# Optimization experiments

Measured on AMD Instinct MI355X. Metric: run time of the kernel, lower is better.

The kernel has to match this reference:

```python
import jax, jax.numpy as jnp
import numpy as np

N_NODES = 50000
E_EDGES = 1600000
D = 256


def setup_inputs() -> dict:
    key = jax.random.key(0)
    ks = jax.random.split(key, 10)
    inp = {
        "x": jax.random.normal(ks[0], (N_NODES, D), dtype=jnp.float32),
        "W0": jax.random.normal(ks[1], (D, D), dtype=jnp.float32) * (1.0 / np.sqrt(D)),
        "W1": jax.random.normal(ks[2], (D, D), dtype=jnp.float32) * (1.0 / np.sqrt(D)),
        "b": jnp.zeros((D,), dtype=jnp.float32),
        "src0": jax.random.randint(ks[3], (E_EDGES,), 0, N_NODES, dtype=jnp.int32),
        "dst0": jax.random.randint(ks[4], (E_EDGES,), 0, N_NODES, dtype=jnp.int32),
        "val0": jax.random.uniform(ks[5], (E_EDGES,), dtype=jnp.float32),
        "src1": jax.random.randint(ks[6], (E_EDGES,), 0, N_NODES, dtype=jnp.int32),
        "dst1": jax.random.randint(ks[7], (E_EDGES,), 0, N_NODES, dtype=jnp.int32),
        "val1": jax.random.uniform(ks[8], (E_EDGES,), dtype=jnp.float32),
    }
    return inp


def _spmm(src, dst, val, dense, num_segments):
    # sparse [N,N] (COO: A[dst, src] = val) @ dense [N,D] -> [N,D]
    # gather rows of dense at src, scale by edge value, scatter-add to dst
    return jax.ops.segment_sum(val[:, None] * dense[src], dst, num_segments=num_segments)


def reference(x, W0, W1, b, src0, dst0, val0, src1, dst1, val1):
    n = x.shape[0]
    # per-support dense GEMM then SpMM, summed over supports (2 supports)
    out = _spmm(src0, dst0, val0, x @ W0, n)
    out = out + _spmm(src1, dst1, val1, x @ W1, n)
    out = out + b  # bias
    return jax.nn.relu(out)  # act = F.relu
```

## Files before the change

kernel.cpp:

```cpp
#include <hip/hip_runtime.h>

#define D 256
#define CAP 64
#define CAP_S 60
#define OVFCAP 16384
#define BCAP 10240
#define CHUNK 8192

typedef __attribute__((ext_vector_type(8))) short short8;
typedef __attribute__((ext_vector_type(4))) float f32x4;

__device__ inline ushort f2bf(float f) {
  unsigned u = __float_as_uint(f);
  unsigned r = (u + 0x7FFF + ((u >> 16) & 1)) >> 16;
  return (ushort)r;
}
__device__ inline float bf_lo(unsigned u) { return __uint_as_float(u << 16); }
__device__ inline float bf_hi(unsigned u) { return __uint_as_float(u & 0xFFFF0000u); }

__global__ __launch_bounds__(256) void prep_kernel(const float* __restrict__ W0,
                                                   const float* __restrict__ W1,
                                                   ushort* __restrict__ Wt0,
                                                   ushort* __restrict__ Wt1,
                                                   int* __restrict__ gz, int ngz) {
  if (blockIdx.x < 128) {
    const int blk = blockIdx.x;
    const float* W = (blk >> 6) ? W1 : W0;
    ushort* Wt = (blk >> 6) ? Wt1 : Wt0;
    __shared__ float t[32][33];
    int tx = threadIdx.x & 31, ty = threadIdx.x >> 5;
    int k0 = (blk & 7) * 32, n0 = ((blk >> 3) & 7) * 32;
    for (int r = ty; r < 32; r += 8)
      t[r][tx] = W[(size_t)(k0 + r) * D + n0 + tx];
    __syncthreads();
    for (int r = ty; r < 32; r += 8)
      Wt[(size_t)(n0 + r) * D + k0 + tx] = f2bf(t[tx][r]);
  } else {
    int nb = gridDim.x - 128;
    for (int i = (blockIdx.x - 128) * 256 + threadIdx.x; i < ngz; i += nb * 256)
      gz[i] = 0;
  }
}

__device__ __forceinline__ void gemm_body(const float* __restrict__ A,
                                          const ushort* __restrict__ Bt,
                                          ushort* __restrict__ C, int M,
                                          int blk, int mtiles) {
  __shared__ ushort As[128 * 40];
  __shared__ ushort Bs[128 * 40];
  const int tid = threadIdx.x;
  const int bm = (blk % mtiles) * 128;
  const int bn = (blk / mtiles) * 128;
  const int wave = tid >> 6, lane = tid & 63;
  const int wm = wave & 1, wn = wave >> 1;
  const int lr = lane & 15;
  const int kg = lane >> 4;
  f32x4 acc[4][4];
#pragma unroll
  for (int m = 0; m < 4; ++m)
#pragma unroll
    for (int n = 0; n < 4; ++n) acc[m][n] = (f32x4){0.f, 0.f, 0.f, 0.f};

  for (int k0 = 0; k0 < D; k0 += 32) {
    __syncthreads();
#pragma unroll
    for (int c = 0; c < 4; ++c) {
      int linear = c * 256 + tid;
      int row = linear >> 3;
      int f4 = linear & 7;
      int gr = bm + row;
      float4 a = (gr < M) ? *(const float4*)(A + (size_t)gr * D + k0 + f4 * 4)
                          : make_float4(0.f, 0.f, 0.f, 0.f);
      ushort4 o;
      o.x = f2bf(a.x); o.y = f2bf(a.y); o.z = f2bf(a.z); o.w = f2bf(a.w);
      *(ushort4*)&As[row * 40 + f4 * 4] = o;
    }
#pragma unroll
    for (int c = 0; c < 2; ++c) {
      int linear = c * 256 + tid;
      int row = linear >> 2;
      int part = linear & 3;
      uint4 w4 = *(const uint4*)(Bt + (size_t)(bn + row) * D + k0 + part * 8);
      *(uint4*)&Bs[row * 40 + part * 8] = w4;
    }
    __syncthreads();
    short8 af[4], bfr[4];
#pragma unroll
    for (int m = 0; m < 4; ++m)
      af[m] = *(const short8*)&As[(wm * 64 + m * 16 + lr) * 40 + kg * 8];
#pragma unroll
    for (int n = 0; n < 4; ++n)
      bfr[n] = *(const short8*)&Bs[(wn * 64 + n * 16 + lr) * 40 + kg * 8];
#pragma unroll
    for (int m = 0; m < 4; ++m)
#pragma unroll
      for (int n = 0; n < 4; ++n)
        acc[m][n] = __builtin_amdgcn_mfma_f32_16x16x32_bf16(af[m], bfr[n], acc[m][n], 0, 0, 0);
  }

#pragma unroll
  for (int m = 0; m < 4; ++m)
#pragma unroll
    for (int j = 0; j < 4; ++j) {
      int gr = bm + wm * 64 + m * 16 + kg * 4 + j;
      if (gr < M) {
#pragma unroll
        for (int n = 0; n < 4; ++n) {
          int gc = bn + wn * 64 + n * 16 + lr;
          C[(size_t)gr * D + gc] = f2bf(acc[m][n][j]);
        }
      }
    }
}

__device__ __forceinline__ void binA_body(const int* __restrict__ src,
                                          const int* __restrict__ dst,
                                          const float* __restrict__ val, int E,
                                          int* __restrict__ gcur,
                                          int2* __restrict__ binned,
                                          int* __restrict__ ovfc, int4* __restrict__ ovf,
                                          int nbkt, int blk) {
  __shared__ int hist[200];
  __shared__ int base[200];
  const int tid = threadIdx.x;
  for (int i = tid; i < nbkt; i += 256) hist[i] = 0;
  __syncthreads();
  const int e0 = blk * CHUNK;
  const int e1 = min(E, e0 + CHUNK);
  for (int e = e0 + tid; e < e1; e += 256)
    atomicAdd(&hist[dst[e] >> 8], 1);
  __syncthreads();
  for (int i = tid; i < nbkt; i += 256) {
    int h = hist[i];
    base[i] = h ? atomicAdd(&gcur[i], h) : 0;
    hist[i] = 0;
  }
  __syncthreads();
  for (int e = e0 + tid; e < e1; e += 256) {
    int d = dst[e];
    int s = src[e];
    int vb = __float_as_int(val[e]);
    int k = d >> 8;
    int pos = base[k] + atomicAdd(&hist[k], 1);
    if (pos < BCAP) {
      binned[(size_t)k * BCAP + pos] = make_int2(((d & 255) << 16) | s, vb);
    } else {
      int o = atomicAdd(ovfc, 1);
      if (o < OVFCAP) ovf[o] = make_int4(d, s, vb, 0);
    }
  }
}

__device__ __forceinline__ void passB_body(const int2* __restrict__ binned,
                                           const int* __restrict__ gcur,
                                           uint* __restrict__ padded,
                                           int* __restrict__ cnt,
                                           int* __restrict__ ovfc, int4* __restrict__ ovf,
                                           int b) {
  __shared__ int lcnt[256];
  __shared__ uint stage[256 * CAP_S];
  const int tid = threadIdx.x;
  lcnt[tid] = 0;
  __syncthreads();
  const int n = min(gcur[b], BCAP);
  const int2* bp = binned + (size_t)b * BCAP;
  for (int i = tid; i < n; i += 256) {
    int2 e = bp[i];
    int dlow = (e.x >> 16) & 255;
    int s = atomicAdd(&lcnt[dlow], 1);
    if (s < CAP_S) {
      float v = __int_as_float(e.y);
      stage[dlow * CAP_S + s] = (uint)(e.x & 0xFFFF) | ((uint)f2bf(v) << 16);
    } else {
      int o = atomicAdd(ovfc, 1);
      if (o < OVFCAP) ovf[o] = make_int4((b << 8) + dlow, e.x & 0xFFFF, e.y, 0);
    }
  }
  __syncthreads();
  const int row = (b << 8) + tid;
  const int written = min(lcnt[tid], CAP_S);
  cnt[row] = written;
  const int nq = (written + 3) >> 2;
  for (int s = written; s < (nq << 2); ++s) stage[tid * CAP_S + s] = 0;
  uint4* dp = (uint4*)(padded + ((size_t)row << 6));
  const uint4* sp = (const uint4*)&stage[tid * CAP_S];
  for (int q = 0; q < nq; ++q) dp[q] = sp[q];
}

__global__ __launch_bounds__(256) void passB(const int2* __restrict__ binned,
                                             const int* __restrict__ gcur,
                                             uint* __restrict__ padded,
                                             int* __restrict__ cnt,
                                             int* __restrict__ ovfc, int4* __restrict__ ovf) {
  passB_body(binned, gcur, padded, cnt, ovfc, ovf, blockIdx.x);
}

__global__ __launch_bounds__(256) void passBoth(
    const int2* __restrict__ binned0, const int* __restrict__ gcur0, uint* __restrict__ padded0,
    int* __restrict__ cnt0, int* __restrict__ ovfc0, int4* __restrict__ ovf0,
    const int2* __restrict__ binned1, const int* __restrict__ gcur1, uint* __restrict__ padded1,
    int* __restrict__ cnt1, int* __restrict__ ovfc1, int4* __restrict__ ovf1, int nbkt) {
  if (blockIdx.x < nbkt)
    passB_body(binned0, gcur0, padded0, cnt0, ovfc0, ovf0, blockIdx.x);
  else
    passB_body(binned1, gcur1, padded1, cnt1, ovfc1, ovf1, blockIdx.x - nbkt);
}

__device__ __forceinline__ void gather_acc(const ushort* __restrict__ H,
                                           const uint* __restrict__ padded,
                                           int row, int c, int lane, float4& acc) {
  const int nc = (c + 3) >> 2;
  if (nc <= 0) return;
  const uint4* ep4 = (const uint4*)(padded + ((size_t)row << 6));
  const uint2* Hl = (const uint2*)H + lane;

  uint2 h0[4], h1[4];
  float v0[4], v1[4];

#define GA_ISSUE(S, J)                                                  \
  do {                                                                  \
    uint4 m = ep4[(J)];                                                 \
    uint ee[4] = {m.x, m.y, m.z, m.w};                                  \
    _Pragma("unroll") for (int k = 0; k < 4; ++k) {                     \
      v##S[k] = __uint_as_float(ee[k] & 0xFFFF0000u);                   \
      h##S[k] = Hl[(size_t)(ee[k] & 0xFFFFu) << 6];                     \
    }                                                                   \
  } while (0)

#define GA_COMP(S)                                                      \
  do {                                                                  \
    _Pragma("unroll") for (int k = 0; k < 4; ++k) {                     \
      acc.x += v##S[k] * bf_lo(h##S[k].x);                              \
      acc.y += v##S[k] * bf_hi(h##S[k].x);                              \
      acc.z += v##S[k] * bf_lo(h##S[k].y);                              \
      acc.w += v##S[k] * bf_hi(h##S[k].y);                              \
    }                                                                   \
  } while (0)

  GA_ISSUE(0, 0);
  if (nc > 1) GA_ISSUE(1, 1);
  int j = 0;
  for (; j + 1 < nc; j += 2) {
    GA_COMP(0);
    if (j + 2 < nc) GA_ISSUE(0, j + 2);
    GA_COMP(1);
    if (j + 3 < nc) GA_ISSUE(1, j + 3);
  }
  if (j < nc) GA_COMP(0);
#undef GA_ISSUE
#undef GA_COMP
}

template <int FINAL>
__device__ __forceinline__ void spmm_body(const ushort* __restrict__ H,
                                          const uint* __restrict__ padded,
                                          const int* __restrict__ cnt,
                                          float* __restrict__ out,
                                          const float* __restrict__ bias, int N,
                                          int blk) {
  const int row = blk * 4 + (threadIdx.x >> 6);
  if (row >= N) return;
  const int lane = threadIdx.x & 63;
  float4 acc = make_float4(0.f, 0.f, 0.f, 0.f);
  gather_acc(H, padded, row, min(cnt[row], CAP), lane, acc);
  float4* op = (float4*)(out + (size_t)row * D) + lane;
  if (FINAL) {
    float4 o = *op;
    float4 bb = ((const float4*)bias)[lane];
    o.x = fmaxf(o.x + acc.x + bb.x, 0.f);
    o.y = fmaxf(o.y + acc.y + bb.y, 0.f);
    o.z = fmaxf(o.z + acc.z + bb.z, 0.f);
    o.w = fmaxf(o.w + acc.w + bb.w, 0.f);
    *op = o;
  } else {
    *op = acc;
  }
}

__global__ __launch_bounds__(256) void spmm_first(const ushort* __restrict__ H,
                                                  const uint* __restrict__ padded,
                                                  const int* __restrict__ cnt,
                                                  float* __restrict__ out,
                                                  const float* __restrict__ bias, int N) {
  spmm_body<0>(H, padded, cnt, out, bias, N, blockIdx.x);
}

__global__ __launch_bounds__(256) void spmm_final(const ushort* __restrict__ H,
                                                  const uint* __restrict__ padded,
                                                  const int* __restrict__ cnt,
                                                  float* __restrict__ out,
                                                  const float* __restrict__ bias, int N) {
  spmm_body<1>(H, padded, cnt, out, bias, N, blockIdx.x);
}

__global__ __launch_bounds__(256) void spmm_fused(
    const ushort* __restrict__ H0, const uint* __restrict__ padded0, const int* __restrict__ cnt0,
    const ushort* __restrict__ H1, const uint* __restrict__ padded1, const int* __restrict__ cnt1,
    float* __restrict__ out, const float* __restrict__ bias,
    const int* __restrict__ rowflag, int N) {
  const int row = blockIdx.x * 4 + (threadIdx.x >> 6);
  if (row >= N) return;
  const int lane = threadIdx.x & 63;
  float4 acc = make_float4(0.f, 0.f, 0.f, 0.f);
  gather_acc(H0, padded0, row, min(cnt0[row], CAP), lane, acc);
  gather_acc(H1, padded1, row, min(cnt1[row], CAP), lane, acc);
  float4* op = (float4*)(out + (size_t)row * D) + lane;
  float4 bb = ((const float4*)bias)[lane];
  float4 base = make_float4(0.f, 0.f, 0.f, 0.f);
  if (rowflag[row]) base = *op;
  float4 o;
  o.x = fmaxf(acc.x + bb.x + base.x, 0.f);
  o.y = fmaxf(acc.y + bb.y + base.y, 0.f);
  o.z = fmaxf(acc.z + bb.z + base.z, 0.f);
  o.w = fmaxf(acc.w + bb.w + base.w, 0.f);
  *op = o;
}

__global__ __launch_bounds__(256) void fatA(
    const float* __restrict__ A, const ushort* __restrict__ Bt0, ushort* __restrict__ H,
    int M, int mtiles,
    const int* __restrict__ src0, const int* __restrict__ dst0, const float* __restrict__ val0,
    int E0, int* __restrict__ gcur0, int2* __restrict__ binned0, int* __restrict__ ovfc0,
    int4* __restrict__ ovf0,
    const int* __restrict__ src1, const int* __restrict__ dst1, const float* __restrict__ val1,
    int E1, int* __restrict__ gcur1, int2* __restrict__ binned1, int* __restrict__ ovfc1,
    int4* __restrict__ ovf1,
    int nbkt, int nbA0, int nbA1) {
  const int bid = blockIdx.x;
  if (bid < nbA0)
    binA_body(src0, dst0, val0, E0, gcur0, binned0, ovfc0, ovf0, nbkt, bid);
  else if (bid < nbA0 + nbA1)
    binA_body(src1, dst1, val1, E1, gcur1, binned1, ovfc1, ovf1, nbkt, bid - nbA0);
  else
    gemm_body(A, Bt0, H, M, bid - nbA0 - nbA1, mtiles);
}

__global__ __launch_bounds__(256) void fatA2(
    const float* __restrict__ A, const ushort* __restrict__ Bt0, const ushort* __restrict__ Bt1,
    ushort* __restrict__ H0, ushort* __restrict__ H1, int M, int mtiles,
    const int* __restrict__ src0, const int* __restrict__ dst0, const float* __restrict__ val0,
    int E0, int* __restrict__ gcur0, int2* __restrict__ binned0, int* __restrict__ ovfc0,
    int4* __restrict__ ovf0,
    const int* __restrict__ src1, const int* __restrict__ dst1, const float* __restrict__ val1,
    int E1, int* __restrict__ gcur1, int2* __restrict__ binned1, int* __restrict__ ovfc1,
    int4* __restrict__ ovf1,
    int nbkt, int nbA0, int nbA1, int NGB) {
  const int bid = blockIdx.x;
  if (bid < nbA0)
    binA_body(src0, dst0, val0, E0, gcur0, binned0, ovfc0, ovf0, nbkt, bid);
  else if (bid < nbA0 + nbA1)
    binA_body(src1, dst1, val1, E1, gcur1, binned1, ovfc1, ovf1, nbkt, bid - nbA0);
  else if (bid < nbA0 + nbA1 + NGB)
    gemm_body(A, Bt0, H0, M, bid - nbA0 - nbA1, mtiles);
  else
    gemm_body(A, Bt1, H1, M, bid - nbA0 - nbA1 - NGB, mtiles);
}

__global__ __launch_bounds__(256) void gemm_plain(const float* __restrict__ A,
                                                  const ushort* __restrict__ Bt,
                                                  ushort* __restrict__ C, int M, int mtiles) {
  gemm_body(A, Bt, C, M, blockIdx.x, mtiles);
}

__global__ void ovf_zero(const int* __restrict__ ovfc0, const int4* __restrict__ ovf0,
                         const int* __restrict__ ovfc1, const int4* __restrict__ ovf1,
                         float* __restrict__ out, int* __restrict__ rowflag) {
  int n0 = min(*ovfc0, OVFCAP);
  int n1 = min(*ovfc1, OVFCAP);
  int w = (blockIdx.x * blockDim.x + threadIdx.x) >> 6;
  int lane = threadIdx.x & 63;
  int nw = (gridDim.x * blockDim.x) >> 6;
  for (int i = w; i < n0 + n1; i += nw) {
    int d = (i < n0) ? ovf0[i].x : ovf1[i - n0].x;
    if (lane == 0) rowflag[d] = 1;
    ((float4*)(out + (size_t)d * D))[lane] = make_float4(0.f, 0.f, 0.f, 0.f);
  }
}

__global__ void overflow_add(const int* __restrict__ ovfc, const int4* __restrict__ ovf,
                             const ushort* __restrict__ H, float* __restrict__ out) {
  int n = min(*ovfc, OVFCAP);
  int w = (blockIdx.x * blockDim.x + threadIdx.x) >> 6;
  int lane = threadIdx.x & 63;
  int nw = (gridDim.x * blockDim.x) >> 6;
  for (int i = w; i < n; i += nw) {
    int4 r = ovf[i];
    uint2 h = *((const uint2*)(H + (size_t)r.y * D) + lane);
    float v = __int_as_float(r.z);
    float* op = out + (size_t)r.x * D + (lane << 2);
    unsafeAtomicAdd(op + 0, v * bf_lo(h.x));
    unsafeAtomicAdd(op + 1, v * bf_hi(h.x));
    unsafeAtomicAdd(op + 2, v * bf_lo(h.y));
    unsafeAtomicAdd(op + 3, v * bf_hi(h.y));
  }
}

extern "C" void kernel_launch(void* const* d_in, const int* in_sizes, int n_in,
                              void* d_out, int out_size, void* d_ws, size_t ws_size,
                              hipStream_t stream) {
  const float* x    = (const float*)d_in[0];
  const float* W0   = (const float*)d_in[1];
  const float* W1   = (const float*)d_in[2];
  const float* b    = (const float*)d_in[3];
  const int*   src0 = (const int*)d_in[4];
  const int*   dst0 = (const int*)d_in[5];
  const float* val0 = (const float*)d_in[6];
  const int*   src1 = (const int*)d_in[7];
  const int*   dst1 = (const int*)d_in[8];
  const float* val1 = (const float*)d_in[9];
  float* out = (float*)d_out;

  const int N  = in_sizes[0] / D;
  const int E0 = in_sizes[4];
  const int E1 = in_sizes[7];
  const int nbkt = (N + 255) >> 8;
  const int nrows = nbkt << 8;

  const int mtiles = (N + 127) / 128;
  const int NGB = mtiles * 2;
  const int nbA0 = (E0 + CHUNK - 1) / CHUNK;
  const int nbA1 = (E1 + CHUNK - 1) / CHUNK;
  const int NPB = (N + 3) / 4;

  size_t off = 0;
  auto alloc = [&](size_t bytes) -> void* {
    void* p = (char*)d_ws + off;
    off = (off + bytes + 255) & ~(size_t)255;
    return p;
  };

  ushort* H0      = (ushort*)alloc((size_t)N * D * 2);
  ushort* H1      = (ushort*)alloc((size_t)N * D * 2);
  ushort* Wt0     = (ushort*)alloc((size_t)D * D * 2);
  ushort* Wt1     = (ushort*)alloc((size_t)D * D * 2);
  int2*   binned0 = (int2*)alloc((size_t)nbkt * BCAP * 8);
  int2*   binned1 = (int2*)alloc((size_t)nbkt * BCAP * 8);
  uint*   padded0 = (uint*)alloc((size_t)nrows * CAP * 4);
  uint*   padded1 = (uint*)alloc((size_t)nrows * CAP * 4);
  int*    cnt0    = (int*)alloc((size_t)nrows * 4);
  int*    cnt1    = (int*)alloc((size_t)nrows * 4);
  int*    gzall   = (int*)alloc((size_t)(2 * nbkt + 2 + nrows) * 4);
  int4*   ovf0    = (int4*)alloc((size_t)OVFCAP * 16);
  int4*   ovf1    = (int4*)alloc((size_t)OVFCAP * 16);
  const bool fused = (off <= ws_size);

  if (!fused) {
    off = 0;
    H0      = (ushort*)alloc((size_t)N * D * 2);
    H1      = H0;
    Wt0     = (ushort*)alloc((size_t)D * D * 2);
    Wt1     = (ushort*)alloc((size_t)D * D * 2);
    binned0 = (int2*)alloc((size_t)nbkt * BCAP * 8);
    binned1 = (int2*)alloc((size_t)nbkt * BCAP * 8);
    padded0 = (uint*)alloc((size_t)nrows * CAP * 4);
    padded1 = (uint*)binned0;
    cnt0    = (int*)alloc((size_t)nrows * 4);
    cnt1    = (int*)alloc((size_t)nrows * 4);
    gzall   = (int*)alloc((size_t)(2 * nbkt + 2) * 4);
    ovf0    = (int4*)alloc((size_t)OVFCAP * 16);
    ovf1    = (int4*)alloc((size_t)OVFCAP * 16);
  }

  int* gcur0   = gzall;
  int* gcur1   = gzall + nbkt;
  int* ovfc0   = gzall + 2 * nbkt;
  int* ovfc1   = gzall + 2 * nbkt + 1;
  int* rowflag = gzall + 2 * nbkt + 2;

  if (fused) {
    prep_kernel<<<160, 256, 0, stream>>>(W0, W1, Wt0, Wt1, gzall, 2 * nbkt + 2 + nrows);
    fatA2<<<nbA0 + nbA1 + 2 * NGB, 256, 0, stream>>>(
        x, Wt0, Wt1, H0, H1, N, mtiles,
        src0, dst0, val0, E0, gcur0, binned0, ovfc0, ovf0,
        src1, dst1, val1, E1, gcur1, binned1, ovfc1, ovf1,
        nbkt, nbA0, nbA1, NGB);
    passBoth<<<2 * nbkt, 256, 0, stream>>>(binned0, gcur0, padded0, cnt0, ovfc0, ovf0,
                                           binned1, gcur1, padded1, cnt1, ovfc1, ovf1, nbkt);
    ovf_zero<<<16, 256, 0, stream>>>(ovfc0, ovf0, ovfc1, ovf1, out, rowflag);
    overflow_add<<<16, 256, 0, stream>>>(ovfc0, ovf0, H0, out);
    overflow_add<<<16, 256, 0, stream>>>(ovfc1, ovf1, H1, out);
    spmm_fused<<<NPB, 256, 0, stream>>>(H0, padded0, cnt0, H1, padded1, cnt1,
                                        out, b, rowflag, N);
  } else {
    prep_kernel<<<160, 256, 0, stream>>>(W0, W1, Wt0, Wt1, gzall, 2 * nbkt + 2);
    fatA<<<nbA0 + nbA1 + NGB, 256, 0, stream>>>(
        x, Wt0, H0, N, mtiles,
        src0, dst0, val0, E0, gcur0, binned0, ovfc0, ovf0,
        src1, dst1, val1, E1, gcur1, binned1, ovfc1, ovf1,
        nbkt, nbA0, nbA1);
    passB<<<nbkt, 256, 0, stream>>>(binned0, gcur0, padded0, cnt0, ovfc0, ovf0);
    spmm_first<<<NPB, 256, 0, stream>>>(H0, padded0, cnt0, out, b, N);
    overflow_add<<<16, 256, 0, stream>>>(ovfc0, ovf0, H0, out);
    gemm_plain<<<NGB, 256, 0, stream>>>(x, Wt1, H0, N, mtiles);
    passB<<<nbkt, 256, 0, stream>>>(binned1, gcur1, padded1, cnt1, ovfc1, ovf1);
    overflow_add<<<16, 256, 0, stream>>>(ovfc1, ovf1, H0, out);
    spmm_final<<<NPB, 256, 0, stream>>>(H0, padded1, cnt1, out, b, N);
  }
}
```

Baseline: 322.1 us.

## Reorder to aggregate-then-transform: SpMM on x, then single concatenated K=512 GEMM

Uses associativity to compute A0·x and A1·x first, sampling bf16 x, writes them side by side into a [N,512] bf16 buffer, then runs one GEMM against the stacked [W0;W1] with bias and ReLU fused into the epilogue. This removes the two separate H GEMMs, the fp32 atomic scatter into out and the rowflag/zeroing passes, and it reuses the binned buffer as Y storage. Overflow edges are now applied by a single-block serial kernel with a read-modify-write in bf16. That adds rounding error and could become a bottleneck if many edges overflow.

```diff
diff --git a/kernel.cpp b/kernel.cpp
--- a/kernel.cpp
+++ b/kernel.cpp
@@ -1,6 +1,7 @@
 #include <hip/hip_runtime.h>
 
 #define D 256
+#define K2 512
 #define CAP 64
 #define CAP_S 60
 #define OVFCAP 16384
@@ -20,97 +21,26 @@
 
 __global__ __launch_bounds__(256) void prep_kernel(const float* __restrict__ W0,
                                                    const float* __restrict__ W1,
-                                                   ushort* __restrict__ Wt0,
-                                                   ushort* __restrict__ Wt1,
+                                                   ushort* __restrict__ Wt,
                                                    int* __restrict__ gz, int ngz) {
   if (blockIdx.x < 128) {
     const int blk = blockIdx.x;
     const float* W = (blk >> 6) ? W1 : W0;
-    ushort* Wt = (blk >> 6) ? Wt1 : Wt0;
+    const int koff = (blk >> 6) ? 256 : 0;
     __shared__ float t[32][33];
     int tx = threadIdx.x & 31, ty = threadIdx.x >> 5;
-    int k0 = (blk & 7) * 32, n0 = ((blk >> 3) & 7) * 32;
+    int b = blk & 63;
+    int k0 = (b & 7) * 32, n0 = (b >> 3) * 32;
     for (int r = ty; r < 32; r += 8)
       t[r][tx] = W[(size_t)(k0 + r) * D + n0 + tx];
     __syncthreads();
     for (int r = ty; r < 32; r += 8)
-      Wt[(size_t)(n0 + r) * D + k0 + tx] = f2bf(t[tx][r]);
+      Wt[(size_t)(n0 + r) * K2 + koff + k0 + tx] = f2bf(t[tx][r]);
   } else {
     int nb = gridDim.x - 128;
     for (int i = (blockIdx.x - 128) * 256 + threadIdx.x; i < ngz; i += nb * 256)
       gz[i] = 0;
   }
-}
-
-__device__ __forceinline__ void gemm_body(const float* __restrict__ A,
-                                          const ushort* __restrict__ Bt,
-                                          ushort* __restrict__ C, int M,
-                                          int blk, int mtiles) {
-  __shared__ ushort As[128 * 40];
-  __shared__ ushort Bs[128 * 40];
-  const int tid = threadIdx.x;
-  const int bm = (blk % mtiles) * 128;
-  const int bn = (blk / mtiles) * 128;
-  const int wave = tid >> 6, lane = tid & 63;
-  const int wm = wave & 1, wn = wave >> 1;
-  const int lr = lane & 15;
-  const int kg = lane >> 4;
-  f32x4 acc[4][4];
-#pragma unroll
-  for (int m = 0; m < 4; ++m)
-#pragma unroll
-    for (int n = 0; n < 4; ++n) acc[m][n] = (f32x4){0.f, 0.f, 0.f, 0.f};
-
-  for (int k0 = 0; k0 < D; k0 += 32) {
-    __syncthreads();
-#pragma unroll
-    for (int c = 0; c < 4; ++c) {
-      int linear = c * 256 + tid;
-      int row = linear >> 3;
-      int f4 = linear & 7;
-      int gr = bm + row;
-      float4 a = (gr < M) ? *(const float4*)(A + (size_t)gr * D + k0 + f4 * 4)
-                          : make_float4(0.f, 0.f, 0.f, 0.f);
-      ushort4 o;
-      o.x = f2bf(a.x); o.y = f2bf(a.y); o.z = f2bf(a.z); o.w = f2bf(a.w);
-      *(ushort4*)&As[row * 40 + f4 * 4] = o;
-    }
-#pragma unroll
-    for (int c = 0; c < 2; ++c) {
-      int linear = c * 256 + tid;
-      int row = linear >> 2;
-      int part = linear & 3;
-      uint4 w4 = *(const uint4*)(Bt + (size_t)(bn + row) * D + k0 + part * 8);
-      *(uint4*)&Bs[row * 40 + part * 8] = w4;
-    }
-    __syncthreads();
-    short8 af[4], bfr[4];
-#pragma unroll
-    for (int m = 0; m < 4; ++m)
-      af[m] = *(const short8*)&As[(wm * 64 + m * 16 + lr) * 40 + kg * 8];
-#pragma unroll
-    for (int n = 0; n < 4; ++n)
-      bfr[n] = *(const short8*)&Bs[(wn * 64 + n * 16 + lr) * 40 + kg * 8];
-#pragma unroll
-    for (int m = 0; m < 4; ++m)
-#pragma unroll
-      for (int n = 0; n < 4; ++n)
-        acc[m][n] = __builtin_amdgcn_mfma_f32_16x16x32_bf16(af[m], bfr[n], acc[m][n], 0, 0, 0);
-  }
-
-#pragma unroll
-  for (int m = 0; m < 4; ++m)
-#pragma unroll
-    for (int j = 0; j < 4; ++j) {
-      int gr = bm + wm * 64 + m * 16 + kg * 4 + j;
-      if (gr < M) {
-#pragma unroll
-        for (int n = 0; n < 4; ++n) {
-          int gc = bn + wn * 64 + n * 16 + lr;
-          C[(size_t)gr * D + gc] = f2bf(acc[m][n][j]);
-        }
-      }
-    }
 }
 
 __device__ __forceinline__ void binA_body(const int* __restrict__ src,
@@ -147,6 +77,31 @@
     } else {
       int o = atomicAdd(ovfc, 1);
       if (o < OVFCAP) ovf[o] = make_int4(d, s, vb, 0);
+    }
+  }
+}
+
+__global__ __launch_bounds__(256) void fat_kernel(
+    const float* __restrict__ x, ushort* __restrict__ Xb, int nq,
+    const int* __restrict__ src0, const int* __restrict__ dst0, const float* __restrict__ val0,
+    int E0, int* __restrict__ gcur0, int2* __restrict__ binned0, int* __restrict__ ovfc0,
+    int4* __restrict__ ovf0,
+    const int* __restrict__ src1, const int* __restrict__ dst1, const float* __restrict__ val1,
+    int E1, int* __restrict__ gcur1, int2* __restrict__ binned1, int* __restrict__ ovfc1,
+    int4* __restrict__ ovf1,
+    int nbkt, int nbA0, int nbA1) {
+  const int bid = blockIdx.x;
+  if (bid < nbA0) {
+    binA_body(src0, dst0, val0, E0, gcur0, binned0, ovfc0, ovf0, nbkt, bid);
+  } else if (bid < nbA0 + nbA1) {
+    binA_body(src1, dst1, val1, E1, gcur1, binned1, ovfc1, ovf1, nbkt, bid - nbA0);
+  } else {
+    const int nxb = gridDim.x - nbA0 - nbA1;
+    for (int i = (bid - nbA0 - nbA1) * 256 + threadIdx.x; i < nq; i += nxb * 256) {
+      float4 v = ((const float4*)x)[i];
+      ushort4 o;
+      o.x = f2bf(v.x); o.y = f2bf(v.y); o.z = f2bf(v.z); o.w = f2bf(v.w);
+      ((ushort4*)Xb)[i] = o;
     }
   }
 }
@@ -187,14 +142,6 @@
   for (int q = 0; q < nq; ++q) dp[q] = sp[q];
 }
 
-__global__ __launch_bounds__(256) void passB(const int2* __restrict__ binned,
-                                             const int* __restrict__ gcur,
-                                             uint* __restrict__ padded,
-                                             int* __restrict__ cnt,
-                                             int* __restrict__ ovfc, int4* __restrict__ ovf) {
-  passB_body(binned, gcur, padded, cnt, ovfc, ovf, blockIdx.x);
-}
-
 __global__ __launch_bounds__(256) void passBoth(
     const int2* __restrict__ binned0, const int* __restrict__ gcur0, uint* __restrict__ padded0,
     int* __restrict__ cnt0, int* __restrict__ ovfc0, int4* __restrict__ ovf0,
@@ -251,148 +198,113 @@
 #undef GA_COMP
 }
 
-template <int FINAL>
-__device__ __forceinline__ void spmm_body(const ushort* __restrict__ H,
-                                          const uint* __restrict__ padded,
-                                          const int* __restrict__ cnt,
-                                          float* __restrict__ out,
-                                          const float* __restrict__ bias, int N,
-                                          int blk) {
-  const int row = blk * 4 + (threadIdx.x >> 6);
-  if (row >= N) return;
-  const int lane = threadIdx.x & 63;
-  float4 acc = make_float4(0.f, 0.f, 0.f, 0.f);
-  gather_acc(H, padded, row, min(cnt[row], CAP), lane, acc);
-  float4* op = (float4*)(out + (size_t)row * D) + lane;
-  if (FINAL) {
-    float4 o = *op;
-    float4 bb = ((const float4*)bias)[lane];
-    o.x = fmaxf(o.x + acc.x + bb.x, 0.f);
-    o.y = fmaxf(o.y + acc.y + bb.y, 0.f);
-    o.z = fmaxf(o.z + acc.z + bb.z, 0.f);
-    o.w = fmaxf(o.w + acc.w + bb.w, 0.f);
-    *op = o;
-  } else {
-    *op = acc;
-  }
-}
-
-__global__ __launch_bounds__(256) void spmm_first(const ushort* __restrict__ H,
-                                                  const uint* __restrict__ padded,
-                                                  const int* __restrict__ cnt,
-                                                  float* __restrict__ out,
-                                                  const float* __restrict__ bias, int N) {
-  spmm_body<0>(H, padded, cnt, out, bias, N, blockIdx.x);
-}
-
-__global__ __launch_bounds__(256) void spmm_final(const ushort* __restrict__ H,
-                                                  const uint* __restrict__ padded,
-                                                  const int* __restrict__ cnt,
-                                                  float* __restrict__ out,
-                                                  const float* __restrict__ bias, int N) {
-  spmm_body<1>(H, padded, cnt, out, bias, N, blockIdx.x);
-}
-
-__global__ __launch_bounds__(256) void spmm_fused(
-    const ushort* __restrict__ H0, const uint* __restrict__ padded0, const int* __restrict__ cnt0,
-    const ushort* __restrict__ H1, const uint* __restrict__ padded1, const int* __restrict__ cnt1,
-    float* __restrict__ out, const float* __restrict__ bias,
-    const int* __restrict__ rowflag, int N) {
+__global__ __launch_bounds__(256) void spmmY(const ushort* __restrict__ Xb,
+                                             const uint* __restrict__ padded0,
+                                             const int* __restrict__ cnt0,
+                                             const uint* __restrict__ padded1,
+                                             const int* __restrict__ cnt1,
+                                             ushort* __restrict__ Y, int N) {
   const int row = blockIdx.x * 4 + (threadIdx.x >> 6);
   if (row >= N) return;
   const int lane = threadIdx.x & 63;
-  float4 acc = make_float4(0.f, 0.f, 0.f, 0.f);
-  gather_acc(H0, padded0, row, min(cnt0[row], CAP), lane, acc);
-  gather_acc(H1, padded1, row, min(cnt1[row], CAP), lane, acc);
-  float4* op = (float4*)(out + (size_t)row * D) + lane;
-  float4 bb = ((const float4*)bias)[lane];
-  float4 base = make_float4(0.f, 0.f, 0.f, 0.f);
-  if (rowflag[row]) base = *op;
-  float4 o;
-  o.x = fmaxf(acc.x + bb.x + base.x, 0.f);
-  o.y = fmaxf(acc.y + bb.y + base.y, 0.f);
-  o.z = fmaxf(acc.z + bb.z + base.z, 0.f);
-  o.w = fmaxf(acc.w + bb.w + base.w, 0.f);
-  *op = o;
-}
-
-__global__ __launch_bounds__(256) void fatA(
-    const float* __restrict__ A, const ushort* __restrict__ Bt0, ushort* __restrict__ H,
-    int M, int mtiles,
-    const int* __restrict__ src0, const int* __restrict__ dst0, const float* __restrict__ val0,
-    int E0, int* __restrict__ gcur0, int2* __restrict__ binned0, int* __restrict__ ovfc0,
-    int4* __restrict__ ovf0,
-    const int* __restrict__ src1, const int* __restrict__ dst1, const float* __restrict__ val1,
-    int E1, int* __restrict__ gcur1, int2* __restrict__ binned1, int* __restrict__ ovfc1,
-    int4* __restrict__ ovf1,
-    int nbkt, int nbA0, int nbA1) {
-  const int bid = blockIdx.x;
-  if (bid < nbA0)
-    binA_body(src0, dst0, val0, E0, gcur0, binned0, ovfc0, ovf0, nbkt, bid);
-  else if (bid < nbA0 + nbA1)
-    binA_body(src1, dst1, val1, E1, gcur1, binned1, ovfc1, ovf1, nbkt, bid - nbA0);
-  else
-    gemm_body(A, Bt0, H, M, bid - nbA0 - nbA1, mtiles);
-}
-
-__global__ __launch_bounds__(256) void fatA2(
-    const float* __restrict__ A, const ushort* __restrict__ Bt0, const ushort* __restrict__ Bt1,
-    ushort* __restrict__ H0, ushort* __restrict__ H1, int M, int mtiles,
-    const int* __restrict__ src0, const int* __restrict__ dst0, const float* __restrict__ val0,
-    int E0, int* __restrict__ gcur0, int2* __restrict__ binned0, int* __restrict__ ovfc0,
-    int4* __restrict__ ovf0,
-    const int* __restrict__ src1, const int* __restrict__ dst1, const float* __restrict__ val1,
-    int E1, int* __restrict__ gcur1, int2* __restrict__ binned1, int* __restrict__ ovfc1,
-    int4* __restrict__ ovf1,
-    int nbkt, int nbA0, int nbA1, int NGB) {
-  const int bid = blockIdx.x;
-  if (bid < nbA0)
-    binA_body(src0, dst0, val0, E0, gcur0, binned0, ovfc0, ovf0, nbkt, bid);
-  else if (bid < nbA0 + nbA1)
-    binA_body(src1, dst1, val1, E1, gcur1, binned1, ovfc1, ovf1, nbkt, bid - nbA0);
-  else if (bid < nbA0 + nbA1 + NGB)
-    gemm_body(A, Bt0, H0, M, bid - nbA0 - nbA1, mtiles);
-  else
-    gemm_body(A, Bt1, H1, M, bid - nbA0 - nbA1 - NGB, mtiles);
-}
-
-__global__ __launch_bounds__(256) void gemm_plain(const float* __restrict__ A,
-                                                  const ushort* __restrict__ Bt,
-                                                  ushort* __restrict__ C, int M, int mtiles) {
-  gemm_body(A, Bt, C, M, blockIdx.x, mtiles);
-}
-
-__global__ void ovf_zero(const int* __restrict__ ovfc0, const int4* __restrict__ ovf0,
-                         const int* __restrict__ ovfc1, const int4* __restrict__ ovf1,
-                         float* __restrict__ out, int* __restrict__ rowflag) {
+  float4 a0 = make_float4(0.f, 0.f, 0.f, 0.f);
+  float4 a1 = make_float4(0.f, 0.f, 0.f, 0.f);
+  gather_acc(Xb, padded0, row, min(cnt0[row], CAP), lane, a0);
+  gather_acc(Xb, padded1, row, min(cnt1[row], CAP), lane, a1);
+  ushort4 o0, o1;
+  o0.x = f2bf(a0.x); o0.y = f2bf(a0.y); o0.z = f2bf(a0.z); o0.w = f2bf(a0.w);
+  o1.x = f2bf(a1.x); o1.y = f2bf(a1.y); o1.z = f2bf(a1.z); o1.w = f2bf(a1.w);
+  *(ushort4*)(Y + (size_t)row * K2 + 4 * lane) = o0;
+  *(ushort4*)(Y + (size_t)row * K2 + 256 + 4 * lane) = o1;
+}
+
+__global__ void ovf_serial(const int* __restrict__ ovfc0, const int4* __restrict__ ovf0,
+                           const int* __restrict__ ovfc1, const int4* __restrict__ ovf1,
+                           const ushort* __restrict__ Xb, ushort* __restrict__ Y) {
   int n0 = min(*ovfc0, OVFCAP);
   int n1 = min(*ovfc1, OVFCAP);
-  int w = (blockIdx.x * blockDim.x + threadIdx.x) >> 6;
-  int lane = threadIdx.x & 63;
-  int nw = (gridDim.x * blockDim.x) >> 6;
-  for (int i = w; i < n0 + n1; i += nw) {
-    int d = (i < n0) ? ovf0[i].x : ovf1[i - n0].x;
-    if (lane == 0) rowflag[d] = 1;
-    ((float4*)(out + (size_t)d * D))[lane] = make_float4(0.f, 0.f, 0.f, 0.f);
-  }
-}
-
-__global__ void overflow_add(const int* __restrict__ ovfc, const int4* __restrict__ ovf,
-                             const ushort* __restrict__ H, float* __restrict__ out) {
-  int n = min(*ovfc, OVFCAP);
-  int w = (blockIdx.x * blockDim.x + threadIdx.x) >> 6;
-  int lane = threadIdx.x & 63;
-  int nw = (gridDim.x * blockDim.x) >> 6;
-  for (int i = w; i < n; i += nw) {
-    int4 r = ovf[i];
-    uint2 h = *((const uint2*)(H + (size_t)r.y * D) + lane);
+  const int tid = threadIdx.x;
+  for (int i = 0; i < n0 + n1; ++i) {
+    int4 r = (i < n0) ? ovf0[i] : ovf1[i - n0];
+    int koff = (i < n0) ? 0 : 256;
     float v = __int_as_float(r.z);
-    float* op = out + (size_t)r.x * D + (lane << 2);
-    unsafeAtomicAdd(op + 0, v * bf_lo(h.x));
-    unsafeAtomicAdd(op + 1, v * bf_hi(h.x));
-    unsafeAtomicAdd(op + 2, v * bf_lo(h.y));
-    unsafeAtomicAdd(op + 3, v * bf_hi(h.y));
-  }
+    size_t yo = (size_t)r.x * K2 + koff + tid;
+    float y = __uint_as_float((uint)Y[yo] << 16);
+    float xv = __uint_as_float((uint)Xb[(size_t)r.y * D + tid] << 16);
+    Y[yo] = f2bf(y + v * xv);
+    __syncthreads();
+  }
+}
+
+__global__ __launch_bounds__(256) void gemm_out(const ushort* __restrict__ Y,
+                                                const ushort* __restrict__ Wt,
+                                                float* __restrict__ out,
+                                                const float* __restrict__ bias,
+                                                int M, int mtiles) {
+  __shared__ ushort As[128 * 40];
+  __shared__ ushort Bs[128 * 40];
+  const int tid = threadIdx.x;
+  const int blk = blockIdx.x;
+  const int bm = (blk % mtiles) * 128;
+  const int bn = (blk / mtiles) * 128;
+  const int wave = tid >> 6, lane = tid & 63;
+  const int wm = wave & 1, wn = wave >> 1;
+  const int lr = lane & 15;
+  const int kg = lane >> 4;
+  f32x4 acc[4][4];
+#pragma unroll
+  for (int m = 0; m < 4; ++m)
+#pragma unroll
+    for (int n = 0; n < 4; ++n) acc[m][n] = (f32x4){0.f, 0.f, 0.f, 0.f};
+
+  for (int k0 = 0; k0 < K2; k0 += 32) {
+    __syncthreads();
+#pragma unroll
+    for (int c = 0; c < 2; ++c) {
+      int linear = c * 256 + tid;
+      int row = linear >> 2;
+      int part = linear & 3;
+      int gr = bm + row;
+      uint4 a4 = make_uint4(0u, 0u, 0u, 0u);
+      if (gr < M) a4 = *(const uint4*)(Y + (size_t)gr * K2 + k0 + part * 8);
+      *(uint4*)&As[row * 40 + part * 8] = a4;
+    }
+#pragma unroll
+    for (int c = 0; c < 2; ++c) {
+      int linear = c * 256 + tid;
+      int row = linear >> 2;
+      int part = linear & 3;
+      uint4 w4 = *(const uint4*)(Wt + (size_t)(bn + row) * K2 + k0 + part * 8);
+      *(uint4*)&Bs[row * 40 + part * 8] = w4;
+    }
+    __syncthreads();
+    short8 af[4], bfr[4];
+#pragma unroll
+    for (int m = 0; m < 4; ++m)
+      af[m] = *(const short8*)&As[(wm * 64 + m * 16 + lr) * 40 + kg * 8];
+#pragma unroll
+    for (int n = 0; n < 4; ++n)
+      bfr[n] = *(const short8*)&Bs[(wn * 64 + n * 16 + lr) * 40 + kg * 8];
+#pragma unroll
+    for (int m = 0; m < 4; ++m)
+#pragma unroll
+      for (int n = 0; n < 4; ++n)
+        acc[m][n] = __builtin_amdgcn_mfma_f32_16x16x32_bf16(af[m], bfr[n], acc[m][n], 0, 0, 0);
+  }
+
+#pragma unroll
+  for (int m = 0; m < 4; ++m)
+#pragma unroll
+    for (int j = 0; j < 4; ++j) {
+      int gr = bm + wm * 64 + m * 16 + kg * 4 + j;
+      if (gr < M) {
+#pragma unroll
+        for (int n = 0; n < 4; ++n) {
+          int gc = bn + wn * 64 + n * 16 + lr;
+          out[(size_t)gr * D + gc] = fmaxf(acc[m][n][j] + bias[gc], 0.f);
+        }
+      }
+    }
 }
 
 extern "C" void kernel_launch(void* const* d_in, const int* in_sizes, int n_in,
@@ -420,6 +332,7 @@
   const int NGB = mtiles * 2;
   const int nbA0 = (E0 + CHUNK - 1) / CHUNK;
   const int nbA1 = (E1 + CHUNK - 1) / CHUNK;
+  const int NXB = 224;
   const int NPB = (N + 3) / 4;
 
   size_t off = 0;
@@ -428,72 +341,33 @@
     off = (off + bytes + 255) & ~(size_t)255;
     return p;
   };
-
-  ushort* H0      = (ushort*)alloc((size_t)N * D * 2);
-  ushort* H1      = (ushort*)alloc((size_t)N * D * 2);
-  ushort* Wt0     = (ushort*)alloc((size_t)D * D * 2);
-  ushort* Wt1     = (ushort*)alloc((size_t)D * D * 2);
-  int2*   binned0 = (int2*)alloc((size_t)nbkt * BCAP * 8);
-  int2*   binned1 = (int2*)alloc((size_t)nbkt * BCAP * 8);
+  ushort* Xb      = (ushort*)alloc((size_t)N * D * 2);
+  ushort* Wt      = (ushort*)alloc((size_t)D * K2 * 2);
   uint*   padded0 = (uint*)alloc((size_t)nrows * CAP * 4);
   uint*   padded1 = (uint*)alloc((size_t)nrows * CAP * 4);
   int*    cnt0    = (int*)alloc((size_t)nrows * 4);
   int*    cnt1    = (int*)alloc((size_t)nrows * 4);
-  int*    gzall   = (int*)alloc((size_t)(2 * nbkt + 2 + nrows) * 4);
+  int*    gzall   = (int*)alloc((size_t)(2 * nbkt + 2) * 4);
   int4*   ovf0    = (int4*)alloc((size_t)OVFCAP * 16);
   int4*   ovf1    = (int4*)alloc((size_t)OVFCAP * 16);
-  const bool fused = (off <= ws_size);
-
-  if (!fused) {
-    off = 0;
-    H0      = (ushort*)alloc((size_t)N * D * 2);
-    H1      = H0;
-    Wt0     = (ushort*)alloc((size_t)D * D * 2);
-    Wt1     = (ushort*)alloc((size_t)D * D * 2);
-    binned0 = (int2*)alloc((size_t)nbkt * BCAP * 8);
-    binned1 = (int2*)alloc((size_t)nbkt * BCAP * 8);
-    padded0 = (uint*)alloc((size_t)nrows * CAP * 4);
-    padded1 = (uint*)binned0;
-    cnt0    = (int*)alloc((size_t)nrows * 4);
-    cnt1    = (int*)alloc((size_t)nrows * 4);
-    gzall   = (int*)alloc((size_t)(2 * nbkt + 2) * 4);
-    ovf0    = (int4*)alloc((size_t)OVFCAP * 16);
-    ovf1    = (int4*)alloc((size_t)OVFCAP * 16);
-  }
-
-  int* gcur0   = gzall;
-  int* gcur1   = gzall + nbkt;
-  int* ovfc0   = gzall + 2 * nbkt;
-  int* ovfc1   = gzall + 2 * nbkt + 1;
-  int* rowflag = gzall + 2 * nbkt + 2;
-
-  if (fused) {
-    prep_kernel<<<160, 256, 0, stream>>>(W0, W1, Wt0, Wt1, gzall, 2 * nbkt + 2 + nrows);
-    fatA2<<<nbA0 + nbA1 + 2 * NGB, 256, 0, stream>>>(
-        x, Wt0, Wt1, H0, H1, N, mtiles,
-        src0, dst0, val0, E0, gcur0, binned0, ovfc0, ovf0,
-        src1, dst1, val1, E1, gcur1, binned1, ovfc1, ovf1,
-        nbkt, nbA0, nbA1, NGB);
-    passBoth<<<2 * nbkt, 256, 0, stream>>>(binned0, gcur0, padded0, cnt0, ovfc0, ovf0,
-                                           binned1, gcur1, padded1, cnt1, ovfc1, ovf1, nbkt);
-    ovf_zero<<<16, 256, 0, stream>>>(ovfc0, ovf0, ovfc1, ovf1, out, rowflag);
-    overflow_add<<<16, 256, 0, stream>>>(ovfc0, ovf0, H0, out);
-    overflow_add<<<16, 256, 0, stream>>>(ovfc1, ovf1, H1, out);
-    spmm_fused<<<NPB, 256, 0, stream>>>(H0, padded0, cnt0, H1, padded1, cnt1,
-                                        out, b, rowflag, N);
-  } else {
-    prep_kernel<<<160, 256, 0, stream>>>(W0, W1, Wt0, Wt1, gzall, 2 * nbkt + 2);
-    fatA<<<nbA0 + nbA1 + NGB, 256, 0, stream>>>(
-        x, Wt0, H0, N, mtiles,
-        src0, dst0, val0, E0, gcur0, binned0, ovfc0, ovf0,
-        src1, dst1, val1, E1, gcur1, binned1, ovfc1, ovf1,
-        nbkt, nbA0, nbA1);
-    passB<<<nbkt, 256, 0, stream>>>(binned0, gcur0, padded0, cnt0, ovfc0, ovf0);
-    spmm_first<<<NPB, 256, 0, stream>>>(H0, padded0, cnt0, out, b, N);
-    overflow_add<<<16, 256, 0, stream>>>(ovfc0, ovf0, H0, out);
-    gemm_plain<<<NGB, 256, 0, stream>>>(x, Wt1, H0, N, mtiles);
-    passB<<<nbkt, 256, 0, stream>>>(binned1, gcur1, padded1, cnt1, ovfc1, ovf1);
-    overflow_add<<<16, 256, 0, stream>>>(ovfc1, ovf1, H0, out);
-    spmm_final<<<NPB, 256, 0, stream>>>(H0, padded1, cnt1, out, b, N);
-  }
-}
+  int2*   binned0 = (int2*)alloc((size_t)nbkt * BCAP * 8);
+  int2*   binned1 = (int2*)alloc((size_t)nbkt * BCAP * 8);
+  ushort* Y       = (ushort*)binned0;
+
+  int* gcur0 = gzall;
+  int* gcur1 = gzall + nbkt;
+  int* ovfc0 = gzall + 2 * nbkt;
+  int* ovfc1 = gzall + 2 * nbkt + 1;
+
+  prep_kernel<<<130, 256, 0, stream>>>(W0, W1, Wt, gzall, 2 * nbkt + 2);
+  fat_kernel<<<nbA0 + nbA1 + NXB, 256, 0, stream>>>(
+      x, Xb, N * D / 4,
+      src0, dst0, val0, E0, gcur0, binned0, ovfc0, ovf0,
+      src1, dst1, val1, E1, gcur1, binned1, ovfc1, ovf1,
+      nbkt, nbA0, nbA1);
+  passBoth<<<2 * nbkt, 256, 0, stream>>>(binned0, gcur0, padded0, cnt0, ovfc0, ovf0,
+                                         binned1, gcur1, padded1, cnt1, ovfc1, ovf1, nbkt);
+  spmmY<<<NPB, 256, 0, stream>>>(Xb, padded0, cnt0, padded1, cnt1, Y, N);
+  ovf_serial<<<1, 256, 0, stream>>>(ovfc0, ovf0, ovfc1, ovf1, Xb, Y);
+  gemm_out<<<NGB, 256, 0, stream>>>(Y, Wt, out, b, N, mtiles);
+}
```

New measurement: 322.1 us. No clear change (-0.0%).
